# Kernel optimization log

Measured on AMD Instinct MI355X. Metric: run time of the kernel, lower is better.

## Reference

```python
import jax, jax.numpy as jnp
import numpy as np

N = 131072          # number of items ranked in one soft_rank call
CAPACITY = 3.0      # self.capcity in the torch module


def _pav_kl(y, w):
    """KL isotonic regression (non-increasing fit) via Pool-Adjacent-Violators.
    Pooled block value = logsumexp(y_block) - logsumexp(w_block).
    Matches torchsort / fast-soft-sort isotonic_kl. Sequential O(N)."""
    n = y.shape[0]

    def push(i, st):
        ly, lw, val, start, ptr = st
        ly = ly.at[ptr].set(y[i])
        lw = lw.at[ptr].set(w[i])
        val = val.at[ptr].set(y[i] - w[i])
        start = start.at[ptr].set(i)
        ptr = ptr + 1

        def cond(s):
            _, _, v, _, p = s
            return (p >= 2) & (v[p - 2] <= v[p - 1])

        def merge(s):
            ly, lw, v, stt, p = s
            ny = jnp.logaddexp(ly[p - 2], ly[p - 1])
            nw = jnp.logaddexp(lw[p - 2], lw[p - 1])
            return (ly.at[p - 2].set(ny), lw.at[p - 2].set(nw),
                    v.at[p - 2].set(ny - nw), stt, p - 1)

        return jax.lax.while_loop(cond, merge, (ly, lw, val, start, ptr))

    z = jnp.zeros((n,), y.dtype)
    st0 = (z, z, z, jnp.full((n,), n, jnp.int32), jnp.int32(0))
    ly, lw, val, start, ptr = jax.lax.fori_loop(0, n, push, st0)
    # invalidate stale stack slots, then map each element to its block value
    start = jnp.where(jnp.arange(n) < ptr, start, n)
    blk = jnp.searchsorted(start, jnp.arange(n), side='right') - 1
    return val[blk]


@jax.custom_vjp
def isotonic_kl(y, w):
    return _pav_kl(y, w)


def _iso_fwd(y, w):
    sol = _pav_kl(y, w)
    return sol, (y, w, sol)


def _iso_bwd(res, g):
    y, w, sol = res
    n = y.shape[0]
    # blocks = maximal runs of constant solution (exact equality by construction)
    blk = jnp.cumsum(jnp.concatenate([jnp.array([True]), sol[1:] != sol[:-1]])) - 1
    gsum = jax.ops.segment_sum(g, blk, num_segments=n)

    def seg_softmax(v):
        m = jax.ops.segment_max(v, blk, num_segments=n)
        lse = jnp.log(jax.ops.segment_sum(jnp.exp(v - m[blk]), blk, num_segments=n)) + m
        return jnp.exp(v - lse[blk])

    return seg_softmax(y) * gsum[blk], -seg_softmax(w) * gsum[blk]


isotonic_kl.defvjp(_iso_fwd, _iso_bwd)


def soft_rank_kl(scores):
    """torchsort.soft_rank(scores[None], regularization='kl'), strength=1, ascending."""
    n = scores.shape[0]
    w_log = jnp.log(jnp.arange(n, 0, -1, dtype=scores.dtype))  # log([n, ..., 1])
    perm = jnp.argsort(-scores)          # descending, stable
    s = scores[perm]
    sol = isotonic_kl(s, w_log)
    inv = jnp.argsort(perm)
    return jnp.exp(s - sol)[inv]


def setup_inputs() -> dict:
    key = jax.random.key(0)
    k = jax.random.split(key, 5)
    x = jax.random.normal(k[0], (N, 1), jnp.float32)
    # torch Linear default init bounds: 1/sqrt(fan_in)
    w1 = jax.random.uniform(k[1], (1, 32), jnp.float32, -1.0, 1.0)
    b1 = jax.random.uniform(k[2], (32,), jnp.float32, -1.0, 1.0)
    lim2 = 1.0 / np.sqrt(32.0)
    w2 = jax.random.uniform(k[3], (32, 1), jnp.float32, -lim2, lim2)
    b2 = jax.random.uniform(k[4], (1,), jnp.float32, -lim2, lim2)
    return {"x": x, "w1": w1, "b1": b1, "w2": w2, "b2": b2}


def reference(x, w1, b1, w2, b2):
    h = jnp.maximum(x @ w1 + b1, 0.0)            # [N, 32]
    scores = (h @ w2 + b2).reshape(-1)           # [N]
    ranks = soft_rank_kl(scores)                 # [N]
    other = jax.lax.stop_gradient(ranks) % CAPACITY
    ranks = (ranks - other) / CAPACITY + 1.0
    return ranks.reshape(-1, 1)
```

## Files before the change

### kernel.cpp

```cpp
#include <hip/hip_runtime.h>
#include <stdint.h>

typedef unsigned int u32;
typedef unsigned long long u64;

#define N_ITEMS 131072
#define NB 131072
#define NSLICE 4
#define MBLK 64
#define BUCK_PER_BLK 2048
#define CH_PER_BLK 32
#define PAD 65
#define REGSLOT 2048
#define FPAD 16
#define FIXSCALE 268435456.0f
#define FIXMASK ((1ull << 46) - 1)


__device__ __forceinline__ float wsumf(int s, int e) {
  return 0.5f * (float)(e - s + 1) * (float)(2 * N_ITEMS - s - e);
}

__device__ __forceinline__ float key_to_score(u32 key) {
  u32 m = ~key;
  u32 u = (m & 0x80000000u) ? (m ^ 0x80000000u) : ~m;
  return __uint_as_float(u);
}

#define LOG2E 1.4426950408889634f
__device__ __forceinline__ float fexp(float x) { return exp2f(x * LOG2E); }

__device__ __forceinline__ u32 bucket_of(u32 key, u32 kmin, u32 kmax) {
  double scale = (double)NB / ((double)(kmax - kmin) + 1.0);
  u32 b = (u32)((double)(key - kmin) * scale);
  return b < NB ? b : (NB - 1);
}

__device__ __forceinline__ float recSY(int2 r) { return __int_as_float(r.y); }

__device__ __forceinline__ u64 agent_ld(const u64* p) {
  return __hip_atomic_load(p, __ATOMIC_RELAXED, __HIP_MEMORY_SCOPE_AGENT);
}

__device__ int merge_step(int2* __restrict__ REC, int slotL, int nL,
                          int slotR, int nR, int gstartR, int gendR,
                          int t, int* shInt) {
  if (t == 0) {
    int a = 0, bb = 0, hasM = 0;
    if (nL > 0 && nR > 0) {
      int2 rL = REC[slotL + nL - 1];
      float SYL = recSY(rL); int stL = rL.x;
      int2 rR = REC[slotR];
      float SYR = recSY(rR);
      int eR = (nR > 1) ? (REC[slotR + 1].x - 1) : (gendR - 1);
      float SWL = wsumf(stL, gstartR - 1);
      float SWR = wsumf(gstartR, eR);
      if (SYL * SWR <= SYR * SWL) {
        hasM = 1;
        float SYM = SYL + SYR; int Ms = stL, Me = eR;
        a = 1; bb = 1;
        for (;;) {
          float SWM = wsumf(Ms, Me);
          if (a < nL) {
            int2 re = REC[slotL + nL - 1 - a];
            float SYe = recSY(re); int ste = re.x;
            float SWe = wsumf(ste, Ms - 1);
            if (SYe * SWM <= SYM * SWe) { SYM += SYe; Ms = ste; ++a; continue; }
          }
          if (bb < nR) {
            int2 rb = REC[slotR + bb];
            float SYb = recSY(rb); int sb = rb.x;
            int eb = (bb + 1 < nR) ? (REC[slotR + bb + 1].x - 1) : (gendR - 1);
            float SWb = wsumf(sb, eb);
            if (SYM * SWb <= SYb * SWM) { SYM += SYb; Me = eb; ++bb; continue; }
          }
          break;
        }
        REC[slotL + nL - a] = make_int2(Ms, __float_as_int(SYM));
      }
    }
    shInt[0] = a; shInt[1] = bb; shInt[2] = hasM;
  }
  __syncthreads();
  int a = shInt[0], bb = shInt[1], hasM = shInt[2];
  int destBase = slotL + nL - a + hasM;
  int srcBase = slotR + bb;
  int ncopy = nR - bb;
  if (destBase != srcBase) {
    for (int off = 0; off < ncopy; off += 2048) {
      int2 v[8];
#pragma unroll
      for (int j = 0; j < 8; ++j) {
        int k2 = off + j * 256 + t;
        if (k2 < ncopy) v[j] = REC[srcBase + k2];
      }
      __syncthreads();
#pragma unroll
      for (int j = 0; j < 8; ++j) {
        int k2 = off + j * 256 + t;
        if (k2 < ncopy) REC[destBase + k2] = v[j];
      }
      __syncthreads();
    }
  }
  __syncthreads();
  return nL - a + hasM + ncopy;
}


__global__ __launch_bounds__(256) void score_key_kernel(
    const float* __restrict__ x,
    const float* __restrict__ w1, const float* __restrict__ b1,
    const float* __restrict__ w2, const float* __restrict__ b2,
    u32* __restrict__ keyRaw, u32* __restrict__ pmin, u32* __restrict__ pmax,
    u64* __restrict__ hist8, u64* __restrict__ flags, u64* __restrict__ grpf) {
  __shared__ u32 wmn[4], wmx[4];
  int t = threadIdx.x;
  int i = blockIdx.x * 256 + t;
  uint4 z = make_uint4(0u, 0u, 0u, 0u);
  ((uint4*)hist8)[i] = z;
  ((uint4*)hist8)[i + N_ITEMS] = z;
  if (i < MBLK) flags[(size_t)i * FPAD] = 0ull;
  if (i < 9) grpf[(size_t)i * FPAD] = 0ull;
  float xv = x[i];
  float s = b2[0];
#pragma unroll
  for (int j = 0; j < 32; ++j) {
    float h = fmaf(xv, w1[j], b1[j]);
    h = fmaxf(h, 0.0f);
    s = fmaf(h, w2[j], s);
  }
  u32 u = __float_as_uint(s);
  u32 m = u ^ ((u & 0x80000000u) ? 0xFFFFFFFFu : 0x80000000u);
  u32 key = ~m;
  keyRaw[i] = key;
  u32 mn = key, mx = key;
#pragma unroll
  for (int off = 32; off > 0; off >>= 1) {
    mn = min(mn, (u32)__shfl_xor((int)mn, off));
    mx = max(mx, (u32)__shfl_xor((int)mx, off));
  }
  if ((t & 63) == 0) { wmn[t >> 6] = mn; wmx[t >> 6] = mx; }
  __syncthreads();
  if (t == 0) {
    mn = min(min(wmn[0], wmn[1]), min(wmn[2], wmn[3]));
    mx = max(max(wmx[0], wmx[1]), max(wmx[2], wmx[3]));
    pmin[blockIdx.x] = mn;
    pmax[blockIdx.x] = mx;
  }
}


__global__ __launch_bounds__(256) void hist_kernel(
    const u32* __restrict__ keyRaw,
    const u32* __restrict__ pmin, const u32* __restrict__ pmax,
    u64* __restrict__ hist8, u32* __restrict__ mm) {
  __shared__ u32 s0[256], s1[256];
  int t = threadIdx.x;
  s0[t] = min(pmin[t], pmin[t + 256]);
  s1[t] = max(pmax[t], pmax[t + 256]);
  __syncthreads();
  for (int off = 128; off > 0; off >>= 1) {
    if (t < off) { s0[t] = min(s0[t], s0[t + off]); s1[t] = max(s1[t], s1[t + off]); }
    __syncthreads();
  }
  u32 kmin = s0[0], kmax = s1[0];
  if (blockIdx.x == 0 && t == 0) { mm[0] = kmin; mm[1] = kmax; }
  int i = blockIdx.x * 256 + t;
  u32 key = keyRaw[i];
  u32 g = bucket_of(key, kmin, kmax);
  float smax = key_to_score(kmin);
  float v = fexp(key_to_score(key) - smax);
  u64 fix = (u64)fmaxf(1.0f, fmaf(v, FIXSCALE, 0.5f));
  size_t slice = (size_t)(blockIdx.x & (NSLICE - 1)) * NB;
  atomicAdd(&hist8[slice + g], (1ull << 46) | fix);
}


__global__ __launch_bounds__(256) void scan_pav_kernel(
    const u64* __restrict__ hist8, u64* __restrict__ flags,
    u32* __restrict__ cdf, int2* __restrict__ REC,
    int* __restrict__ cnt2, u32* __restrict__ rstart) {
  __shared__ u32 vals[BUCK_PER_BLK + 1];
  __shared__ float seL[BUCK_PER_BLK];
  __shared__ int   rST[CH_PER_BLK * PAD];
  __shared__ float rSY[CH_PER_BLK * PAD];
  __shared__ u32 wsum[4];
  __shared__ u32 regS[65];
  __shared__ int lcnt[CH_PER_BLK];
  __shared__ int ca[16], cb[16], cM[16];
  int t = threadIdx.x, b = blockIdx.x;
  int B0 = b * BUCK_PER_BLK;
  for (int q = 0; q < 8; ++q) {
    int ii = q * 256 + t;
    u64 acc = 0;
#pragma unroll
    for (int c = 0; c < NSLICE; ++c) acc += hist8[(size_t)c * NB + B0 + ii];
    vals[ii] = (u32)(acc >> 46);
    seL[ii] = (float)(acc & FIXMASK) * (1.0f / FIXSCALE);
  }
  __syncthreads();
  u32 loc[8]; u32 s = 0;
  for (int q = 0; q < 8; ++q) { loc[q] = s; s += vals[t * 8 + q]; }
  u32 inc = s;
#pragma unroll
  for (int off = 1; off < 64; off <<= 1) {
    u32 o2 = (u32)__shfl_up((int)inc, off);
    if ((t & 63) >= off) inc += o2;
  }
  if ((t & 63) == 63) wsum[t >> 6] = inc;
  __syncthreads();
  u32 w = (u32)(t >> 6);
  u32 woff = 0;
  if (w > 0) woff += wsum[0];
  if (w > 1) woff += wsum[1];
  if (w > 2) woff += wsum[2];
  u32 total = wsum[0] + wsum[1] + wsum[2] + wsum[3];
  u32 texcl = woff + inc - s;
  if (t == 0) atomicExch(&flags[(size_t)b * FPAD], (1ull << 32) | (u64)total);
  if (t < 64) {
    u64 f;
    do { f = agent_ld(&flags[(size_t)t * FPAD]); } while ((u32)(f >> 32) == 0u);
    u32 v = (u32)f, inc2 = v;
#pragma unroll
    for (int off = 1; off < 64; off <<= 1) {
      u32 o2 = (u32)__shfl_up((int)inc2, off);
      if (t >= off) inc2 += o2;
    }
    regS[t] = inc2 - v;
    if (t == 63) regS[64] = inc2;
  }
  __syncthreads();
  u32 exclu = regS[b];
  u32 tbase = texcl + exclu;
  u32 eb8[8];
  for (int q = 0; q < 8; ++q) { eb8[q] = tbase + loc[q]; vals[t * 8 + q] = eb8[q]; }
  {
    uint4* c4 = (uint4*)(cdf + B0 + t * 8);
    c4[0] = make_uint4(eb8[0], eb8[1], eb8[2], eb8[3]);
    c4[1] = make_uint4(eb8[4], eb8[5], eb8[6], eb8[7]);
  }
  if (t == 255) vals[BUCK_PER_BLK] = exclu + total;
  if (b == 0 && t < 65) rstart[t] = regS[t];
  __syncthreads();
  if (t < CH_PER_BLK) {
    int base = t * PAD;
    int ptr = 0; bool have = false;
    float syT = 0.0f; int stT = 0;
    for (int k = 0; k < 64; ++k) {
      u32 cs = vals[t * 64 + k], ce = vals[t * 64 + k + 1];
      if (ce == cs) continue;
      float syC = seL[t * 64 + k];
      int stC = (int)cs, eC = (int)ce - 1;
      while (have) {
        float SWc = wsumf(stC, eC);
        float SWt = wsumf(stT, stC - 1);
        if (!(syT * SWc <= syC * SWt)) break;
        syC += syT; stC = stT;
        if (ptr == 0) { have = false; break; }
        --ptr;
        stT = rST[base + ptr]; syT = rSY[base + ptr];
      }
      if (have) { rST[base + ptr] = stT; rSY[base + ptr] = syT; ++ptr; }
      stT = stC; syT = syC; have = true;
    }
    if (have) { rST[base + ptr] = stT; rSY[base + ptr] = syT; ++ptr; }
    lcnt[t] = ptr;
  }
  __syncthreads();
  for (int j = 0; j < 5; ++j) {
    int P = CH_PER_BLK >> (j + 1);
    if (t < P) {
      int p = t;
      int kL = p << (j + 1), kR = kL + (1 << j);
      int slotL = kL * PAD, slotR = kR * PAD;
      int nL = lcnt[kL], nR = lcnt[kR];
      int a = 0, bb = 0, hasM = 0;
      if (nL > 0 && nR > 0) {
        int gstartR = (int)vals[kR * 64];
        int gendR   = (int)vals[(kR + (1 << j)) * 64];
        float SYL = rSY[slotL + nL - 1]; int stL = rST[slotL + nL - 1];
        float SYR = rSY[slotR];
        int eR = (nR > 1) ? (rST[slotR + 1] - 1) : (gendR - 1);
        float SWL = wsumf(stL, gstartR - 1);
        float SWR = wsumf(gstartR, eR);
        if (SYL * SWR <= SYR * SWL) {
          hasM = 1;
          float SYM = SYL + SYR; int Ms = stL, Me = eR;
          a = 1; bb = 1;
          for (;;) {
            float SWM = wsumf(Ms, Me);
            if (a < nL) {
              float SYe = rSY[slotL + nL - 1 - a]; int ste = rST[slotL + nL - 1 - a];
              float SWe = wsumf(ste, Ms - 1);
              if (SYe * SWM <= SYM * SWe) { SYM += SYe; Ms = ste; ++a; continue; }
            }
            if (bb < nR) {
              float SYb = rSY[slotR + bb]; int sb = rST[slotR + bb];
              int eb = (bb + 1 < nR) ? (rST[slotR + bb + 1] - 1) : (gendR - 1);
              float SWb = wsumf(sb, eb);
              if (SYM * SWb <= SYb * SWM) { SYM += SYb; Me = eb; ++bb; continue; }
            }
            break;
          }
          rST[slotL + nL - a] = Ms; rSY[slotL + nL - a] = SYM;
        }
      }
      ca[p] = a; cb[p] = bb; cM[p] = hasM;
    }
    __syncthreads();
    {
      int wv = t >> 6, lane = t & 63;
      for (int p = wv; p < P; p += 4) {
        int kL = p << (j + 1), kR = kL + (1 << j);
        int nL = lcnt[kL], nR = lcnt[kR];
        int a = ca[p], bb = cb[p], hasM = cM[p];
        int destBase = kL * PAD + nL - a + hasM;
        int srcBase = kR * PAD + bb;
        int ncopy = nR - bb;
        for (int off = 0; off < ncopy; off += 64) {
          int k2 = off + lane; bool act = k2 < ncopy;
          int vt = 0; float vs = 0.f;
          if (act) { vt = rST[srcBase + k2]; vs = rSY[srcBase + k2]; }
          if (act) { rST[destBase + k2] = vt; rSY[destBase + k2] = vs; }
        }
      }
    }
    __syncthreads();
    if (t < P) {
      int p = t; int kL = p << (j + 1), kR = kL + (1 << j);
      lcnt[kL] = lcnt[kL] - ca[p] + cM[p] + (lcnt[kR] - cb[p]);
    }
    __syncthreads();
  }
  int n = lcnt[0];
  for (int k = t; k < n; k += 256)
    REC[(size_t)b * REGSLOT + k] = make_int2(rST[k], __float_as_int(rSY[k]));
  if (t == 0) cnt2[b] = n;
}


__global__ __launch_bounds__(256) void merge_kernel(
    int2* __restrict__ REC, int* __restrict__ cnt2,
    const u32* __restrict__ rstart, u64* __restrict__ grpf) {
  __shared__ int shInt[4];
  __shared__ int gcnt[8];
  __shared__ u32 rs[65];
  __shared__ int pcnt[8];
  int t = threadIdx.x, b = blockIdx.x;
  if (t < 8) gcnt[t] = cnt2[b * 8 + t];
  if (t < 65) rs[t] = rstart[t];
  __syncthreads();
  int nL = gcnt[0];
  int slotL = (b * 8) * REGSLOT;
  for (int k = 1; k < 8; ++k) {
    int nR = gcnt[k];
    int slotR = (b * 8 + k) * REGSLOT;
    nL = merge_step(REC, slotL, nL, slotR, nR,
                    (int)rs[b * 8 + k], (int)rs[b * 8 + k + 1], t, shInt);
  }
  if (t == 0) { __threadfence(); atomicExch(&grpf[(size_t)b * FPAD], (1ull << 32) | (u64)(u32)nL); }
  if (b == 0) {
    if (t < 7) {
      u64 f;
      do { f = agent_ld(&grpf[(size_t)(1 + t) * FPAD]); } while ((u32)(f >> 32) == 0u);
      pcnt[1 + t] = (int)(u32)f;
    }
    __syncthreads();
    __threadfence();
    for (int k = 1; k < 8; ++k) {
      int nR = pcnt[k];
      int slotR = (k * 8) * REGSLOT;
      nL = merge_step(REC, 0, nL, slotR, nR,
                      (int)rs[k * 8], (int)rs[k * 8 + 8], t, shInt);
    }
    if (t == 0) cnt2[0] = nL;
  }
}


__global__ __launch_bounds__(256) void out_kernel(
    const u32* __restrict__ keyRaw, const u32* __restrict__ mm,
    const u32* __restrict__ cdf, const int2* __restrict__ REC,
    const int* __restrict__ cnt2, float* __restrict__ out) {
  __shared__ int   rST[CH_PER_BLK * PAD];
  __shared__ float rSY[CH_PER_BLK * PAD];
  int t = threadIdx.x;
  int i = blockIdx.x * 256 + t;
  int m = cnt2[0];
  u32 kmin = mm[0], kmax = mm[1];
  u32 key = keyRaw[i];
  float smax = key_to_score(kmin);
  u32 g = bucket_of(key, kmin, kmax);
  int p = (int)cdf[g];
  bool useL = (m <= CH_PER_BLK * PAD);
  if (useL) {
    for (int k = t; k < m; k += 256) {
      int2 r = REC[k];
      rST[k] = r.x; rSY[k] = __int_as_float(r.y);
    }
  }
  __syncthreads();
  int lo = 0, hi = m - 1;
  if (useL) {
    while (lo < hi) {
      int mid = (lo + hi + 1) >> 1;
      if (rST[mid] <= p) lo = mid; else hi = mid - 1;
    }
    int s0 = rST[lo];
    int e0 = (lo + 1 < m) ? (rST[lo + 1] - 1) : (N_ITEMS - 1);
    float SW = wsumf(s0, e0);
    float rank = fexp(key_to_score(key) - smax) * SW / rSY[lo];
    out[i] = floorf(rank * (1.0f / 3.0f)) + 1.0f;
  } else {
    while (lo < hi) {
      int mid = (lo + hi + 1) >> 1;
      if (REC[mid].x <= p) lo = mid; else hi = mid - 1;
    }
    int2 r = REC[lo];
    int s0 = r.x;
    int e0 = (lo + 1 < m) ? (REC[lo + 1].x - 1) : (N_ITEMS - 1);
    float SW = wsumf(s0, e0);
    float rank = fexp(key_to_score(key) - smax) * SW / recSY(r);
    out[i] = floorf(rank * (1.0f / 3.0f)) + 1.0f;
  }
}


extern "C" void kernel_launch(void* const* d_in, const int* in_sizes, int n_in,
                              void* d_out, int out_size, void* d_ws, size_t ws_size,
                              hipStream_t stream) {
  const float* x  = (const float*)d_in[0];
  const float* w1 = (const float*)d_in[1];
  const float* b1 = (const float*)d_in[2];
  const float* w2 = (const float*)d_in[3];
  const float* b2 = (const float*)d_in[4];
  float* out = (float*)d_out;

  char* ws = (char*)d_ws;
  size_t o = 0;
  u32* mm     = (u32*)(ws + o); o += 64;
  u32* pmin   = (u32*)(ws + o); o += (size_t)512 * 4;
  u32* pmax   = (u32*)(ws + o); o += (size_t)512 * 4;
  u32* cdf    = (u32*)(ws + o); o += (size_t)(NB + 4) * 4;
  u32* rstart = (u32*)(ws + o); o += (size_t)(MBLK + 4) * 4;
  u32* keyRaw = (u32*)(ws + o); o += (size_t)N_ITEMS * 4;
  int2* REC   = (int2*)(ws + o); o += (size_t)N_ITEMS * 8;
  int* cnt2   = (int*)(ws + o);  o += (size_t)MBLK * 4;
  u64* hist8  = (u64*)(ws + o); o += (size_t)NSLICE * NB * 8;
  u64* flags  = (u64*)(ws + o); o += (size_t)MBLK * FPAD * 8;
  u64* grpf   = (u64*)(ws + o); o += (size_t)9 * FPAD * 8;

  score_key_kernel<<<512, 256, 0, stream>>>(x, w1, b1, w2, b2, keyRaw,
                                            pmin, pmax, hist8, flags, grpf);
  hist_kernel<<<512, 256, 0, stream>>>(keyRaw, pmin, pmax, hist8, mm);
  scan_pav_kernel<<<MBLK, 256, 0, stream>>>(hist8, flags, cdf, REC, cnt2, rstart);
  merge_kernel<<<8, 256, 0, stream>>>(REC, cnt2, rstart, grpf);
  out_kernel<<<512, 256, 0, stream>>>(keyRaw, mm, cdf, REC, cnt2, out);
}
```

Measured before the change: 116.8 us.

## Fuse merge and output kernels with flag-based handoff and LDS-resident merging

Result: slower. 148.4 us (+27.0%).

```diff
diff --git a/kernel.cpp b/kernel.cpp
--- a/kernel.cpp
+++ b/kernel.cpp
@@ -13,6 +13,8 @@
 #define PAD 65
 #define REGSLOT 2048
 #define FPAD 16
+#define CAPL 2176
+#define CAPS 2048
 #define FIXSCALE 268435456.0f
 #define FIXMASK ((1ull << 46) - 1)
 
@@ -107,13 +109,49 @@
   return nL - a + hasM + ncopy;
 }
 
+__device__ void lds_cascade(int* mST, float* mSY, int n,
+                            const int* sST, const float* sSY, int nR,
+                            int gstartR, int gendR, int* shInt) {
+  int a = 0, bb = 0, hasM = 0;
+  if (n > 0 && nR > 0) {
+    float SYL = mSY[n - 1]; int stL = mST[n - 1];
+    float SYR = sSY[0];
+    int eR = (nR > 1) ? (sST[1] - 1) : (gendR - 1);
+    float SWL = wsumf(stL, gstartR - 1);
+    float SWR = wsumf(gstartR, eR);
+    if (SYL * SWR <= SYR * SWL) {
+      hasM = 1;
+      float SYM = SYL + SYR; int Ms = stL, Me = eR;
+      a = 1; bb = 1;
+      for (;;) {
+        float SWM = wsumf(Ms, Me);
+        if (a < n) {
+          float SYe = mSY[n - 1 - a]; int ste = mST[n - 1 - a];
+          float SWe = wsumf(ste, Ms - 1);
+          if (SYe * SWM <= SYM * SWe) { SYM += SYe; Ms = ste; ++a; continue; }
+        }
+        if (bb < nR) {
+          float SYb = sSY[bb]; int sb = sST[bb];
+          int eb = (bb + 1 < nR) ? (sST[bb + 1] - 1) : (gendR - 1);
+          float SWb = wsumf(sb, eb);
+          if (SYM * SWb <= SYb * SWM) { SYM += SYb; Me = eb; ++bb; continue; }
+        }
+        break;
+      }
+      mST[n - a] = Ms; mSY[n - a] = SYM;
+    }
+  }
+  shInt[0] = a; shInt[1] = bb; shInt[2] = hasM;
+}
+
 
 __global__ __launch_bounds__(256) void score_key_kernel(
     const float* __restrict__ x,
     const float* __restrict__ w1, const float* __restrict__ b1,
     const float* __restrict__ w2, const float* __restrict__ b2,
     u32* __restrict__ keyRaw, u32* __restrict__ pmin, u32* __restrict__ pmax,
-    u64* __restrict__ hist8, u64* __restrict__ flags, u64* __restrict__ grpf) {
+    u64* __restrict__ hist8, u64* __restrict__ flags, u64* __restrict__ grpf,
+    u64* __restrict__ ownf) {
   __shared__ u32 wmn[4], wmx[4];
   int t = threadIdx.x;
   int i = blockIdx.x * 256 + t;
@@ -121,7 +159,8 @@
   ((uint4*)hist8)[i] = z;
   ((uint4*)hist8)[i + N_ITEMS] = z;
   if (i < MBLK) flags[(size_t)i * FPAD] = 0ull;
-  if (i < 9) grpf[(size_t)i * FPAD] = 0ull;
+  if (i < 8) grpf[(size_t)i * FPAD] = 0ull;
+  if (i < 512) ownf[(size_t)i * FPAD] = 0ull;
   float xv = x[i];
   float s = b2[0];
 #pragma unroll
@@ -340,64 +379,171 @@
 }
 
 
-__global__ __launch_bounds__(256) void merge_kernel(
-    int2* __restrict__ REC, int* __restrict__ cnt2,
-    const u32* __restrict__ rstart, u64* __restrict__ grpf) {
+__global__ __launch_bounds__(256) void merge_out_kernel(
+    int2* __restrict__ REC, const int* __restrict__ cnt2,
+    const u32* __restrict__ rstart, u64* __restrict__ grpf, u64* __restrict__ ownf,
+    const u32* __restrict__ keyRaw, const u32* __restrict__ mm,
+    const u32* __restrict__ cdf, float* __restrict__ out) {
+  __shared__ int   mST[CAPL];
+  __shared__ float mSY[CAPL];
+  __shared__ int   sST[CAPS];
+  __shared__ float sSY[CAPS];
+  __shared__ u32 rs[65];
+  __shared__ int gcnt[8];
+  __shared__ int pcnt[8];
   __shared__ int shInt[4];
-  __shared__ int gcnt[8];
-  __shared__ u32 rs[65];
-  __shared__ int pcnt[8];
   int t = threadIdx.x, b = blockIdx.x;
-  if (t < 8) gcnt[t] = cnt2[b * 8 + t];
-  if (t < 65) rs[t] = rstart[t];
-  __syncthreads();
-  int nL = gcnt[0];
-  int slotL = (b * 8) * REGSLOT;
-  for (int k = 1; k < 8; ++k) {
-    int nR = gcnt[k];
-    int slotR = (b * 8 + k) * REGSLOT;
-    nL = merge_step(REC, slotL, nL, slotR, nR,
-                    (int)rs[b * 8 + k], (int)rs[b * 8 + k + 1], t, shInt);
-  }
-  if (t == 0) { __threadfence(); atomicExch(&grpf[(size_t)b * FPAD], (1ull << 32) | (u64)(u32)nL); }
+  int i = b * 256 + t;
+
+  int p_ = 0; float oexp = 0.0f;
+  u32 kmin = mm[0], kmax = mm[1];
+  float smax = key_to_score(kmin);
+  u32 okey;
+  bool inLds = false;
+  int n = 0;
+
+  if (b >= 8) {
+    okey = keyRaw[i];
+    u32 g = bucket_of(okey, kmin, kmax);
+    p_ = (int)cdf[g];
+    oexp = fexp(key_to_score(okey) - smax);
+  } else {
+    if (t < 8) gcnt[t] = cnt2[b * 8 + t];
+    if (t < 65) rs[t] = rstart[t];
+    __syncthreads();
+    int total8 = 0;
+#pragma unroll
+    for (int k = 0; k < 8; ++k) total8 += gcnt[k];
+    n = gcnt[0];
+    int slotL = (b * 8) * REGSLOT;
+    if (total8 <= CAPL) {
+      inLds = true;
+      for (int k2 = t; k2 < n; k2 += 256) {
+        int2 r = REC[slotL + k2]; mST[k2] = r.x; mSY[k2] = __int_as_float(r.y);
+      }
+      __syncthreads();
+      for (int k = 1; k < 8; ++k) {
+        int nR = gcnt[k];
+        int slotR = (b * 8 + k) * REGSLOT;
+        for (int k2 = t; k2 < nR; k2 += 256) {
+          int2 r = REC[slotR + k2]; sST[k2] = r.x; sSY[k2] = __int_as_float(r.y);
+        }
+        __syncthreads();
+        if (t == 0) lds_cascade(mST, mSY, n, sST, sSY, nR,
+                                (int)rs[b * 8 + k], (int)rs[b * 8 + k + 1], shInt);
+        __syncthreads();
+        int a = shInt[0], bb = shInt[1], hasM = shInt[2];
+        int destBase = n - a + hasM;
+        int ncopy = nR - bb;
+        for (int k2 = t; k2 < ncopy; k2 += 256) {
+          mST[destBase + k2] = sST[bb + k2]; mSY[destBase + k2] = sSY[bb + k2];
+        }
+        __syncthreads();
+        n = destBase + ncopy;
+      }
+      if (b != 0) {
+        for (int k2 = t; k2 < n; k2 += 256)
+          REC[slotL + k2] = make_int2(mST[k2], __float_as_int(mSY[k2]));
+      }
+    } else {
+      for (int k = 1; k < 8; ++k) {
+        int nR = gcnt[k];
+        int slotR = (b * 8 + k) * REGSLOT;
+        n = merge_step(REC, slotL, n, slotR, nR,
+                       (int)rs[b * 8 + k], (int)rs[b * 8 + k + 1], t, shInt);
+      }
+    }
+    __syncthreads();
+    if (b != 0) {
+      if (t == 0) { __threadfence(); atomicExch(&grpf[(size_t)b * FPAD], (1ull << 32) | (u64)(u32)n); }
+      okey = keyRaw[i];
+      u32 g = bucket_of(okey, kmin, kmax);
+      p_ = (int)cdf[g];
+      oexp = fexp(key_to_score(okey) - smax);
+    } else {
+      if (t < 7) {
+        u64 f;
+        do { f = agent_ld(&grpf[(size_t)(1 + t) * FPAD]); } while ((u32)(f >> 32) == 0u);
+        pcnt[1 + t] = (int)(u32)f;
+      }
+      __syncthreads();
+      __threadfence();
+      int totalF = n;
+      for (int k = 1; k < 8; ++k) totalF += pcnt[k];
+      if (totalF <= CAPL) {
+        if (!inLds) {
+          for (int k2 = t; k2 < n; k2 += 256) {
+            int2 r = REC[k2]; mST[k2] = r.x; mSY[k2] = __int_as_float(r.y);
+          }
+          __syncthreads();
+          inLds = true;
+        }
+        for (int k = 1; k < 8; ++k) {
+          int nR = pcnt[k];
+          int slotR = (k * 8) * REGSLOT;
+          for (int k2 = t; k2 < nR; k2 += 256) {
+            int2 r = REC[slotR + k2]; sST[k2] = r.x; sSY[k2] = __int_as_float(r.y);
+          }
+          __syncthreads();
+          if (t == 0) lds_cascade(mST, mSY, n, sST, sSY, nR,
+                                  (int)rs[k * 8], (int)rs[k * 8 + 8], shInt);
+          __syncthreads();
+          int a = shInt[0], bb = shInt[1], hasM = shInt[2];
+          int destBase = n - a + hasM;
+          int ncopy = nR - bb;
+          for (int k2 = t; k2 < ncopy; k2 += 256) {
+            mST[destBase + k2] = sST[bb + k2]; mSY[destBase + k2] = sSY[bb + k2];
+          }
+          __syncthreads();
+          n = destBase + ncopy;
+        }
+        for (int k2 = t; k2 < n; k2 += 256)
+          REC[k2] = make_int2(mST[k2], __float_as_int(mSY[k2]));
+      } else {
+        inLds = false;
+        for (int k = 1; k < 8; ++k) {
+          int nR = pcnt[k];
+          int slotR = (k * 8) * REGSLOT;
+          n = merge_step(REC, 0, n, slotR, nR,
+                         (int)rs[k * 8], (int)rs[k * 8 + 8], t, shInt);
+        }
+      }
+      __syncthreads();
+      if (t == 0) __threadfence();
+      __syncthreads();
+      {
+        u64 v = (1ull << 32) | (u64)(u32)n;
+        for (int k2 = t; k2 < 512; k2 += 256) atomicExch(&ownf[(size_t)k2 * FPAD], v);
+      }
+      okey = keyRaw[i];
+      u32 g = bucket_of(okey, kmin, kmax);
+      p_ = (int)cdf[g];
+      oexp = fexp(key_to_score(okey) - smax);
+    }
+  }
+
+  int m;
   if (b == 0) {
-    if (t < 7) {
+    m = n;
+  } else {
+    if (t == 0) {
       u64 f;
-      do { f = agent_ld(&grpf[(size_t)(1 + t) * FPAD]); } while ((u32)(f >> 32) == 0u);
-      pcnt[1 + t] = (int)(u32)f;
+      do {
+        f = agent_ld(&ownf[(size_t)b * FPAD]);
+        if ((f >> 32) == 0ull) __builtin_amdgcn_s_sleep(2);
+      } while ((f >> 32) == 0ull);
+      shInt[3] = (int)(u32)f;
     }
     __syncthreads();
     __threadfence();
-    for (int k = 1; k < 8; ++k) {
-      int nR = pcnt[k];
-      int slotR = (k * 8) * REGSLOT;
-      nL = merge_step(REC, 0, nL, slotR, nR,
-                      (int)rs[k * 8], (int)rs[k * 8 + 8], t, shInt);
-    }
-    if (t == 0) cnt2[0] = nL;
-  }
-}
-
-
-__global__ __launch_bounds__(256) void out_kernel(
-    const u32* __restrict__ keyRaw, const u32* __restrict__ mm,
-    const u32* __restrict__ cdf, const int2* __restrict__ REC,
-    const int* __restrict__ cnt2, float* __restrict__ out) {
-  __shared__ int   rST[CH_PER_BLK * PAD];
-  __shared__ float rSY[CH_PER_BLK * PAD];
-  int t = threadIdx.x;
-  int i = blockIdx.x * 256 + t;
-  int m = cnt2[0];
-  u32 kmin = mm[0], kmax = mm[1];
-  u32 key = keyRaw[i];
-  float smax = key_to_score(kmin);
-  u32 g = bucket_of(key, kmin, kmax);
-  int p = (int)cdf[g];
-  bool useL = (m <= CH_PER_BLK * PAD);
-  if (useL) {
+    m = shInt[3];
+    inLds = false;
+  }
+  bool useL = (m <= CAPL);
+  if (useL && !inLds) {
     for (int k = t; k < m; k += 256) {
       int2 r = REC[k];
-      rST[k] = r.x; rSY[k] = __int_as_float(r.y);
+      mST[k] = r.x; mSY[k] = __int_as_float(r.y);
     }
   }
   __syncthreads();
@@ -405,23 +551,23 @@
   if (useL) {
     while (lo < hi) {
       int mid = (lo + hi + 1) >> 1;
-      if (rST[mid] <= p) lo = mid; else hi = mid - 1;
-    }
-    int s0 = rST[lo];
-    int e0 = (lo + 1 < m) ? (rST[lo + 1] - 1) : (N_ITEMS - 1);
+      if (mST[mid] <= p_) lo = mid; else hi = mid - 1;
+    }
+    int s0 = mST[lo];
+    int e0 = (lo + 1 < m) ? (mST[lo + 1] - 1) : (N_ITEMS - 1);
     float SW = wsumf(s0, e0);
-    float rank = fexp(key_to_score(key) - smax) * SW / rSY[lo];
+    float rank = oexp * SW / mSY[lo];
     out[i] = floorf(rank * (1.0f / 3.0f)) + 1.0f;
   } else {
     while (lo < hi) {
       int mid = (lo + hi + 1) >> 1;
-      if (REC[mid].x <= p) lo = mid; else hi = mid - 1;
+      if (REC[mid].x <= p_) lo = mid; else hi = mid - 1;
     }
     int2 r = REC[lo];
     int s0 = r.x;
     int e0 = (lo + 1 < m) ? (REC[lo + 1].x - 1) : (N_ITEMS - 1);
     float SW = wsumf(s0, e0);
-    float rank = fexp(key_to_score(key) - smax) * SW / recSY(r);
+    float rank = oexp * SW / recSY(r);
     out[i] = floorf(rank * (1.0f / 3.0f)) + 1.0f;
   }
 }
@@ -449,12 +595,13 @@
   int* cnt2   = (int*)(ws + o);  o += (size_t)MBLK * 4;
   u64* hist8  = (u64*)(ws + o); o += (size_t)NSLICE * NB * 8;
   u64* flags  = (u64*)(ws + o); o += (size_t)MBLK * FPAD * 8;
-  u64* grpf   = (u64*)(ws + o); o += (size_t)9 * FPAD * 8;
+  u64* grpf   = (u64*)(ws + o); o += (size_t)8 * FPAD * 8;
+  u64* ownf   = (u64*)(ws + o); o += (size_t)512 * FPAD * 8;
 
   score_key_kernel<<<512, 256, 0, stream>>>(x, w1, b1, w2, b2, keyRaw,
-                                            pmin, pmax, hist8, flags, grpf);
+                                            pmin, pmax, hist8, flags, grpf, ownf);
   hist_kernel<<<512, 256, 0, stream>>>(keyRaw, pmin, pmax, hist8, mm);
   scan_pav_kernel<<<MBLK, 256, 0, stream>>>(hist8, flags, cdf, REC, cnt2, rstart);
-  merge_kernel<<<8, 256, 0, stream>>>(REC, cnt2, rstart, grpf);
-  out_kernel<<<512, 256, 0, stream>>>(keyRaw, mm, cdf, REC, cnt2, out);
-}
+  merge_out_kernel<<<512, 256, 0, stream>>>(REC, cnt2, rstart, grpf, ownf,
+                                            keyRaw, mm, cdf, out);
+}
```

## Fuse merge kernel into scan-PAV kernel with flag-based tree merge

Applied to the files above, without the earlier changes.

After: 116.6 us. Within noise of the previous version (-0.2%).

```diff
diff --git a/kernel.cpp b/kernel.cpp
--- a/kernel.cpp
+++ b/kernel.cpp
@@ -13,6 +13,7 @@
 #define PAD 65
 #define REGSLOT 2048
 #define FPAD 16
+#define CAPO 4096
 #define FIXSCALE 268435456.0f
 #define FIXMASK ((1ull << 46) - 1)
 
@@ -113,7 +114,8 @@
     const float* __restrict__ w1, const float* __restrict__ b1,
     const float* __restrict__ w2, const float* __restrict__ b2,
     u32* __restrict__ keyRaw, u32* __restrict__ pmin, u32* __restrict__ pmax,
-    u64* __restrict__ hist8, u64* __restrict__ flags, u64* __restrict__ grpf) {
+    u64* __restrict__ hist8, u64* __restrict__ flags, u64* __restrict__ flag2,
+    u64* __restrict__ grpf) {
   __shared__ u32 wmn[4], wmx[4];
   int t = threadIdx.x;
   int i = blockIdx.x * 256 + t;
@@ -121,7 +123,8 @@
   ((uint4*)hist8)[i] = z;
   ((uint4*)hist8)[i + N_ITEMS] = z;
   if (i < MBLK) flags[(size_t)i * FPAD] = 0ull;
-  if (i < 9) grpf[(size_t)i * FPAD] = 0ull;
+  if (i < MBLK) flag2[(size_t)i * FPAD] = 0ull;
+  if (i < 8) grpf[(size_t)i * FPAD] = 0ull;
   float xv = x[i];
   float s = b2[0];
 #pragma unroll
@@ -177,10 +180,10 @@
 }
 
 
-__global__ __launch_bounds__(256) void scan_pav_kernel(
-    const u64* __restrict__ hist8, u64* __restrict__ flags,
-    u32* __restrict__ cdf, int2* __restrict__ REC,
-    int* __restrict__ cnt2, u32* __restrict__ rstart) {
+__global__ __launch_bounds__(256) void scan_pav_merge_kernel(
+    const u64* __restrict__ hist8, u64* __restrict__ flags, u64* __restrict__ flag2,
+    u64* __restrict__ grpf, u32* __restrict__ cdf, int2* __restrict__ REC,
+    int* __restrict__ cnt2) {
   __shared__ u32 vals[BUCK_PER_BLK + 1];
   __shared__ float seL[BUCK_PER_BLK];
   __shared__ int   rST[CH_PER_BLK * PAD];
@@ -189,6 +192,8 @@
   __shared__ u32 regS[65];
   __shared__ int lcnt[CH_PER_BLK];
   __shared__ int ca[16], cb[16], cM[16];
+  __shared__ int shInt[4];
+  __shared__ int pm[8];
   int t = threadIdx.x, b = blockIdx.x;
   int B0 = b * BUCK_PER_BLK;
   for (int q = 0; q < 8; ++q) {
@@ -241,7 +246,6 @@
     c4[1] = make_uint4(eb8[4], eb8[5], eb8[6], eb8[7]);
   }
   if (t == 255) vals[BUCK_PER_BLK] = exclu + total;
-  if (b == 0 && t < 65) rstart[t] = regS[t];
   __syncthreads();
   if (t < CH_PER_BLK) {
     int base = t * PAD;
@@ -336,46 +340,33 @@
   int n = lcnt[0];
   for (int k = t; k < n; k += 256)
     REC[(size_t)b * REGSLOT + k] = make_int2(rST[k], __float_as_int(rSY[k]));
-  if (t == 0) cnt2[b] = n;
-}
-
-
-__global__ __launch_bounds__(256) void merge_kernel(
-    int2* __restrict__ REC, int* __restrict__ cnt2,
-    const u32* __restrict__ rstart, u64* __restrict__ grpf) {
-  __shared__ int shInt[4];
-  __shared__ int gcnt[8];
-  __shared__ u32 rs[65];
-  __shared__ int pcnt[8];
-  int t = threadIdx.x, b = blockIdx.x;
-  if (t < 8) gcnt[t] = cnt2[b * 8 + t];
-  if (t < 65) rs[t] = rstart[t];
-  __syncthreads();
-  int nL = gcnt[0];
-  int slotL = (b * 8) * REGSLOT;
-  for (int k = 1; k < 8; ++k) {
-    int nR = gcnt[k];
-    int slotR = (b * 8 + k) * REGSLOT;
-    nL = merge_step(REC, slotL, nL, slotR, nR,
-                    (int)rs[b * 8 + k], (int)rs[b * 8 + k + 1], t, shInt);
-  }
-  if (t == 0) { __threadfence(); atomicExch(&grpf[(size_t)b * FPAD], (1ull << 32) | (u64)(u32)nL); }
-  if (b == 0) {
-    if (t < 7) {
-      u64 f;
-      do { f = agent_ld(&grpf[(size_t)(1 + t) * FPAD]); } while ((u32)(f >> 32) == 0u);
-      pcnt[1 + t] = (int)(u32)f;
-    }
-    __syncthreads();
-    __threadfence();
-    for (int k = 1; k < 8; ++k) {
-      int nR = pcnt[k];
-      int slotR = (k * 8) * REGSLOT;
-      nL = merge_step(REC, 0, nL, slotR, nR,
-                      (int)rs[k * 8], (int)rs[k * 8 + 8], t, shInt);
-    }
-    if (t == 0) cnt2[0] = nL;
-  }
+  __syncthreads();
+  if (t == 0) { __threadfence(); atomicExch(&flag2[(size_t)b * FPAD], (1ull << 32) | (u64)(u32)n); }
+  if ((b & 7) != 0) return;
+  if (t < 7) {
+    u64 f;
+    do { f = agent_ld(&flag2[(size_t)(b + 1 + t) * FPAD]); } while ((u32)(f >> 32) == 0u);
+    pm[1 + t] = (int)(u32)f;
+  }
+  __syncthreads();
+  __threadfence();
+  int nL = n;
+  for (int k = 1; k < 8; ++k)
+    nL = merge_step(REC, b * REGSLOT, nL, (b + k) * REGSLOT, pm[k],
+                    (int)regS[b + k], (int)regS[b + k + 1], t, shInt);
+  if (t == 0) { __threadfence(); atomicExch(&grpf[(size_t)(b >> 3) * FPAD], (1ull << 32) | (u64)(u32)nL); }
+  if (b != 0) return;
+  if (t < 7) {
+    u64 f;
+    do { f = agent_ld(&grpf[(size_t)(1 + t) * FPAD]); } while ((u32)(f >> 32) == 0u);
+    pm[1 + t] = (int)(u32)f;
+  }
+  __syncthreads();
+  __threadfence();
+  for (int k = 1; k < 8; ++k)
+    nL = merge_step(REC, 0, nL, (k * 8) * REGSLOT, pm[k],
+                    (int)regS[k * 8], (int)regS[k * 8 + 8], t, shInt);
+  if (t == 0) cnt2[0] = nL;
 }
 
 
@@ -383,8 +374,8 @@
     const u32* __restrict__ keyRaw, const u32* __restrict__ mm,
     const u32* __restrict__ cdf, const int2* __restrict__ REC,
     const int* __restrict__ cnt2, float* __restrict__ out) {
-  __shared__ int   rST[CH_PER_BLK * PAD];
-  __shared__ float rSY[CH_PER_BLK * PAD];
+  __shared__ int   rST[CAPO];
+  __shared__ float rSY[CAPO];
   int t = threadIdx.x;
   int i = blockIdx.x * 256 + t;
   int m = cnt2[0];
@@ -393,7 +384,7 @@
   float smax = key_to_score(kmin);
   u32 g = bucket_of(key, kmin, kmax);
   int p = (int)cdf[g];
-  bool useL = (m <= CH_PER_BLK * PAD);
+  bool useL = (m <= CAPO);
   if (useL) {
     for (int k = t; k < m; k += 256) {
       int2 r = REC[k];
@@ -443,18 +434,18 @@
   u32* pmin   = (u32*)(ws + o); o += (size_t)512 * 4;
   u32* pmax   = (u32*)(ws + o); o += (size_t)512 * 4;
   u32* cdf    = (u32*)(ws + o); o += (size_t)(NB + 4) * 4;
-  u32* rstart = (u32*)(ws + o); o += (size_t)(MBLK + 4) * 4;
   u32* keyRaw = (u32*)(ws + o); o += (size_t)N_ITEMS * 4;
   int2* REC   = (int2*)(ws + o); o += (size_t)N_ITEMS * 8;
   int* cnt2   = (int*)(ws + o);  o += (size_t)MBLK * 4;
   u64* hist8  = (u64*)(ws + o); o += (size_t)NSLICE * NB * 8;
   u64* flags  = (u64*)(ws + o); o += (size_t)MBLK * FPAD * 8;
-  u64* grpf   = (u64*)(ws + o); o += (size_t)9 * FPAD * 8;
+  u64* flag2  = (u64*)(ws + o); o += (size_t)MBLK * FPAD * 8;
+  u64* grpf   = (u64*)(ws + o); o += (size_t)8 * FPAD * 8;
 
   score_key_kernel<<<512, 256, 0, stream>>>(x, w1, b1, w2, b2, keyRaw,
-                                            pmin, pmax, hist8, flags, grpf);
+                                            pmin, pmax, hist8, flags, flag2, grpf);
   hist_kernel<<<512, 256, 0, stream>>>(keyRaw, pmin, pmax, hist8, mm);
-  scan_pav_kernel<<<MBLK, 256, 0, stream>>>(hist8, flags, cdf, REC, cnt2, rstart);
-  merge_kernel<<<8, 256, 0, stream>>>(REC, cnt2, rstart, grpf);
+  scan_pav_merge_kernel<<<MBLK, 256, 0, stream>>>(hist8, flags, flag2, grpf,
+                                                  cdf, REC, cnt2);
   out_kernel<<<512, 256, 0, stream>>>(keyRaw, mm, cdf, REC, cnt2, out);
 }
```
